# Optimization experiments

Hardware: AMD Instinct MI355X
Metric: run time of the kernel (lower is better)

The kernel has to match this reference:

```python
import jax, jax.numpy as jnp
import numpy as np

N = 100000   # nodes
E = 1250000  # edges
D = 64       # in = hidden = out channels
LN_EPS = 1e-5
L2_EPS = 1e-12


def setup_inputs() -> dict:
    key = jax.random.key(0)
    ks = jax.random.split(key, 16)
    s = 1.0 / np.sqrt(D)
    inp = {
        "x": jax.random.normal(ks[0], (N, D), jnp.float32),
        "edge_index": jax.random.randint(ks[1], (2, E), 0, N, dtype=jnp.int64),
    }
    for i in range(3):  # SAGEConv i: out = mean_aggr @ Wl + bl + x @ Wr
        inp[f"Wl{i}"] = jax.random.normal(ks[2 + 2 * i], (D, D), jnp.float32) * s
        inp[f"bl{i}"] = jnp.zeros((D,), jnp.float32)
        inp[f"Wr{i}"] = jax.random.normal(ks[3 + 2 * i], (D, D), jnp.float32) * s
    for i in range(2):  # LayerNorm after layers 0,1
        inp[f"g{i}"] = jnp.ones((D,), jnp.float32)
        inp[f"b{i}"] = jnp.zeros((D,), jnp.float32)
    return inp


def _sage_conv(x, src, dst, Wl, bl, Wr):
    # PyG SAGEConv(aggr='mean'): lin_l(mean of neighbor msgs) + lin_r(x)
    agg = jax.ops.segment_sum(x[src], dst, num_segments=N)          # [N, D]
    deg = jax.ops.segment_sum(jnp.ones((src.shape[0],), x.dtype), dst, num_segments=N)
    mean = agg / jnp.maximum(deg, 1.0)[:, None]
    return mean @ Wl + bl + x @ Wr


def _layer_norm(h, g, b):
    mu = jnp.mean(h, axis=-1, keepdims=True)
    var = jnp.mean((h - mu) ** 2, axis=-1, keepdims=True)
    return (h - mu) * jax.lax.rsqrt(var + LN_EPS) * g + b


def reference(x, edge_index, Wl0, bl0, Wr0, Wl1, bl1, Wr1, Wl2, bl2, Wr2, g0, b0, g1, b1):
    src, dst = edge_index[0], edge_index[1]
    Ws = [(Wl0, bl0, Wr0), (Wl1, bl1, Wr1), (Wl2, bl2, Wr2)]
    lns = [(g0, b0), (g1, b1)]
    h = x
    for i in range(3):
        res = h  # residual projections are Identity (equal dims)
        h = _sage_conv(h, src, dst, *Ws[i])
        if i < 2:
            h = _layer_norm(h, *lns[i])
            h = jax.nn.relu(h)
            h = h + res
            # dropout is identity in eval mode
        else:
            h = h + res
    # F.normalize(p=2, dim=1)
    nrm = jnp.sqrt(jnp.sum(h * h, axis=1, keepdims=True))
    return h / jnp.maximum(nrm, L2_EPS)
```

## Files before the change

kernel.cpp:

```cpp
#include <hip/hip_runtime.h>

#define DD   64
#define BSH  9
#define BNODES 512
#define BCAPSH 13

typedef unsigned int uint32;
typedef __attribute__((ext_vector_type(8))) short short8;
typedef __attribute__((ext_vector_type(4))) float f32x4;

__device__ __forceinline__ unsigned short f2bf_rne(float f) {
    uint32 u = __float_as_uint(f);
    u += 0x7fffu + ((u >> 16) & 1u);
    return (unsigned short)(u >> 16);
}
__device__ __forceinline__ float bf_lo(uint32 w) { return __uint_as_float(w << 16); }
__device__ __forceinline__ float bf_hi(uint32 w) { return __uint_as_float(w & 0xffff0000u); }
__device__ __forceinline__ float bf2f(unsigned short s) {
    return __uint_as_float(((uint32)s) << 16);
}

__global__ __launch_bounds__(256) void cvt_kernel(
    const float* __restrict__ x, unsigned short* __restrict__ xb, int n4,
    int* __restrict__ gCnt,
    const float* __restrict__ Wl0, const float* __restrict__ Wr0,
    const float* __restrict__ Wl1, const float* __restrict__ Wr1,
    const float* __restrict__ Wl2, const float* __restrict__ Wr2,
    unsigned short* __restrict__ wtg) {
    const int gid = blockIdx.x * 256 + threadIdx.x;
    if (blockIdx.x == 0) gCnt[threadIdx.x] = 0;
    if (gid < 3 * 2 * DD * DD) {
        int layer = gid >> 13;
        int idx   = gid & 8191;
        int k = idx >> 6, c = idx & 63;
        const float* Wsrc;
        if (layer == 0)      Wsrc = (k < DD) ? Wl0 : Wr0;
        else if (layer == 1) Wsrc = (k < DD) ? Wl1 : Wr1;
        else                 Wsrc = (k < DD) ? Wl2 : Wr2;
        float v = Wsrc[(k & (DD - 1)) * DD + c];
        wtg[layer * 8192 + c * 128 + k] = f2bf_rne(v);
    }
    if (gid < n4) {
        float4 v = ((const float4*)x)[gid];
        ushort4 p;
        p.x = f2bf_rne(v.x); p.y = f2bf_rne(v.y);
        p.z = f2bf_rne(v.z); p.w = f2bf_rne(v.w);
        ((ushort4*)xb)[gid] = p;
    }
}

__global__ __launch_bounds__(1024) void bucket_kernel(const int* __restrict__ src,
                                                      const int* __restrict__ dst,
                                                      int* __restrict__ gCnt,
                                                      int2* __restrict__ buf, int E) {
    __shared__ int ldsCnt[256];
    __shared__ int base[256];
    const int t = threadIdx.x;
    if (t < 256) ldsCnt[t] = 0;
    __syncthreads();

    const int e0 = blockIdx.x * 4096;
    int bk[4], rk[4], sv[4], dv[4];
#pragma unroll
    for (int k = 0; k < 4; ++k) {
        int e = e0 + k * 1024 + t;
        bk[k] = -1;
        if (e < E) {
            dv[k] = dst[e];
            sv[k] = src[e];
            bk[k] = dv[k] >> BSH;
            rk[k] = atomicAdd(&ldsCnt[bk[k]], 1);
        }
    }
    __syncthreads();
    if (t < 256 && ldsCnt[t] > 0) base[t] = atomicAdd(&gCnt[t], ldsCnt[t]);
    __syncthreads();
#pragma unroll
    for (int k = 0; k < 4; ++k) {
        if (bk[k] >= 0) {
            int pos = (bk[k] << BCAPSH) + base[bk[k]] + rk[k];
            buf[pos] = make_int2(sv[k], dv[k]);
        }
    }
}

__global__ __launch_bounds__(512) void csr_build(const int2* __restrict__ buf,
                                                 const int* __restrict__ gCnt,
                                                 int* __restrict__ offsets,
                                                 int* __restrict__ csr, int N, int E) {
    __shared__ int c1[BNODES];
    __shared__ int s2[BNODES];
    __shared__ int sw[16];
    const int b = blockIdx.x;
    const int t = threadIdx.x;
    const int lane = t & 63;
    const int w = t >> 6;

    int gv = (t < 256 && t < b) ? gCnt[t] : 0;
#pragma unroll
    for (int d = 1; d < 64; d <<= 1) gv += __shfl_xor(gv, d, 64);
    if (lane == 0) sw[w] = gv;
    c1[t] = 0;
    __syncthreads();
    int base = 0;
#pragma unroll
    for (int i = 0; i < 8; ++i) base += sw[i];

    const int cnt = gCnt[b];
    const int2* bb = buf + ((size_t)b << BCAPSH);
    for (int i = t; i < cnt; i += 512) atomicAdd(&c1[bb[i].y & (BNODES - 1)], 1);
    __syncthreads();

    int v = c1[t];
    int x = v;
#pragma unroll
    for (int d = 1; d < 64; d <<= 1) {
        int y = __shfl_up(x, d, 64);
        if (lane >= d) x += y;
    }
    if (lane == 63) sw[8 + w] = x;
    __syncthreads();
    int woff = 0;
    for (int i = 0; i < w; ++i) woff += sw[8 + i];
    int excl = x + woff - v;

    const int node = (b << BSH) + t;
    if (node < N) offsets[node] = base + excl;
    if (b == 0 && t == 0) offsets[N] = E;

    s2[t] = excl;
    c1[t] = 0;
    __syncthreads();

    for (int i = t; i < cnt; i += 512) {
        int2 e = bb[i];
        int d = e.y & (BNODES - 1);
        int r = atomicAdd(&c1[d], 1);
        csr[base + s2[d] + r] = e.x;
    }
}

__global__ __launch_bounds__(256, 4) void gather_mean(
    const unsigned short* __restrict__ hbin,
    const int* __restrict__ offsets,
    const int* __restrict__ csr,
    unsigned short* __restrict__ mean,
    int N) {
    const int grp  = threadIdx.x >> 3;
    const int q    = threadIdx.x & 7;
    const int node = blockIdx.x * 32 + grp;
    if (node >= N) return;

    const int off0 = offsets[node];
    const int off1 = offsets[node + 1];
    const int deg  = off1 - off0;

    float a0 = 0.f, a1 = 0.f, a2 = 0.f, a3 = 0.f,
          a4 = 0.f, a5 = 0.f, a6 = 0.f, a7 = 0.f;
#pragma unroll 1
    for (int j = off0; j < off1; j += 8) {
        uint4 v[8];
#pragma unroll
        for (int s = 0; s < 8; ++s) {
            uint4 tt = make_uint4(0u, 0u, 0u, 0u);
            int idx = j + s;
            if (idx < off1) {
                int sn = __builtin_nontemporal_load(&csr[idx]);
                tt = ((const uint4*)(hbin + (size_t)sn * DD))[q];
            }
            v[s] = tt;
        }
#pragma unroll
        for (int s = 0; s < 8; ++s) {
            a0 += bf_lo(v[s].x); a1 += bf_hi(v[s].x);
            a2 += bf_lo(v[s].y); a3 += bf_hi(v[s].y);
            a4 += bf_lo(v[s].z); a5 += bf_hi(v[s].z);
            a6 += bf_lo(v[s].w); a7 += bf_hi(v[s].w);
        }
    }
    float invd = 1.0f / fmaxf((float)deg, 1.0f);
    uint4 wv;
    wv.x = (uint32)f2bf_rne(a0 * invd) | ((uint32)f2bf_rne(a1 * invd) << 16);
    wv.y = (uint32)f2bf_rne(a2 * invd) | ((uint32)f2bf_rne(a3 * invd) << 16);
    wv.z = (uint32)f2bf_rne(a4 * invd) | ((uint32)f2bf_rne(a5 * invd) << 16);
    wv.w = (uint32)f2bf_rne(a6 * invd) | ((uint32)f2bf_rne(a7 * invd) << 16);
    *(uint4*)(mean + (size_t)node * DD + q * 8) = wv;
}

template <int MODE>
__global__ __launch_bounds__(256, 4) void sage_xform(
    const unsigned short* __restrict__ hbin,
    const unsigned short* __restrict__ mean,
    const unsigned short* __restrict__ wt,
    const float* __restrict__ bl,
    const float* __restrict__ g,
    const float* __restrict__ bta,
    unsigned short* __restrict__ hbout,
    float* __restrict__ out,
    int N) {
    const int t = threadIdx.x;
    const int nbase = blockIdx.x * 64;
    const int wave = t >> 6;
    const int lane = t & 63;
    const int quad = lane >> 4;
    const int n16  = lane & 15;
    const int lbase = wave * 16;

    const int arow = min(nbase + lbase + n16, N - 1);
    short8 af[4];
    af[0] = *(const short8*)(mean + (size_t)arow * DD + quad * 8);
    af[1] = *(const short8*)(mean + (size_t)arow * DD + 32 + quad * 8);
    af[2] = *(const short8*)(hbin + (size_t)arow * DD + quad * 8);
    af[3] = *(const short8*)(hbin + (size_t)arow * DD + 32 + quad * 8);

    f32x4 acc[4];
#pragma unroll
    for (int j = 0; j < 4; ++j) {
        float bv = bl[j * 16 + n16];
        acc[j] = (f32x4){bv, bv, bv, bv};
    }
#pragma unroll
    for (int s = 0; s < 4; ++s) {
#pragma unroll
        for (int j = 0; j < 4; ++j) {
            short8 bf = *(const short8*)(wt + (j * 16 + n16) * 128 + s * 32 + quad * 8);
            acc[j] = __builtin_amdgcn_mfma_f32_16x16x32_bf16(af[s], bf, acc[j], 0, 0, 0);
        }
    }

    float sg[4], sb[4];
    if (MODE == 0) {
#pragma unroll
        for (int j = 0; j < 4; ++j) { sg[j] = g[j * 16 + n16]; sb[j] = bta[j * 16 + n16]; }
    }

#pragma unroll
    for (int i = 0; i < 4; ++i) {
        const int lrow = lbase + quad * 4 + i;
        const int rr   = nbase + lrow;
        const int rrc  = min(rr, N - 1);
        float res[4];
#pragma unroll
        for (int j = 0; j < 4; ++j)
            res[j] = bf2f(hbin[(size_t)rrc * DD + j * 16 + n16]);
        float o[4];
        if (MODE == 0) {
            float s4 = acc[0][i] + acc[1][i] + acc[2][i] + acc[3][i];
            s4 += __shfl_xor(s4, 1, 64);
            s4 += __shfl_xor(s4, 2, 64);
            s4 += __shfl_xor(s4, 4, 64);
            s4 += __shfl_xor(s4, 8, 64);
            float mu = s4 * (1.0f / 64.0f);
            float d0 = acc[0][i] - mu, d1 = acc[1][i] - mu,
                  d2 = acc[2][i] - mu, d3 = acc[3][i] - mu;
            float qq = d0 * d0 + d1 * d1 + d2 * d2 + d3 * d3;
            qq += __shfl_xor(qq, 1, 64);
            qq += __shfl_xor(qq, 2, 64);
            qq += __shfl_xor(qq, 4, 64);
            qq += __shfl_xor(qq, 8, 64);
            float rstd = rsqrtf(qq * (1.0f / 64.0f) + 1e-5f);
            o[0] = fmaxf(d0 * rstd * sg[0] + sb[0], 0.f) + res[0];
            o[1] = fmaxf(d1 * rstd * sg[1] + sb[1], 0.f) + res[1];
            o[2] = fmaxf(d2 * rstd * sg[2] + sb[2], 0.f) + res[2];
            o[3] = fmaxf(d3 * rstd * sg[3] + sb[3], 0.f) + res[3];
        } else {
            o[0] = acc[0][i] + res[0];
            o[1] = acc[1][i] + res[1];
            o[2] = acc[2][i] + res[2];
            o[3] = acc[3][i] + res[3];
            float qq = o[0] * o[0] + o[1] * o[1] + o[2] * o[2] + o[3] * o[3];
            qq += __shfl_xor(qq, 1, 64);
            qq += __shfl_xor(qq, 2, 64);
            qq += __shfl_xor(qq, 4, 64);
            qq += __shfl_xor(qq, 8, 64);
            float inv = 1.0f / fmaxf(sqrtf(qq), 1e-12f);
            o[0] *= inv; o[1] *= inv; o[2] *= inv; o[3] *= inv;
        }
        if (rr < N) {
#pragma unroll
            for (int j = 0; j < 4; ++j) {
                if (MODE == 0)
                    hbout[(size_t)rr * DD + j * 16 + n16] = f2bf_rne(o[j]);
                else
                    out[(size_t)rr * DD + j * 16 + n16] = o[j];
            }
        }
    }
}

extern "C" void kernel_launch(void* const* d_in, const int* in_sizes, int n_in,
                              void* d_out, int out_size, void* d_ws, size_t ws_size,
                              hipStream_t stream) {
    const float* x   = (const float*)d_in[0];
    const int*   ei  = (const int*)d_in[1];
    const float* Wl0 = (const float*)d_in[2];
    const float* bl0 = (const float*)d_in[3];
    const float* Wr0 = (const float*)d_in[4];
    const float* Wl1 = (const float*)d_in[5];
    const float* bl1 = (const float*)d_in[6];
    const float* Wr1 = (const float*)d_in[7];
    const float* Wl2 = (const float*)d_in[8];
    const float* bl2 = (const float*)d_in[9];
    const float* Wr2 = (const float*)d_in[10];
    const float* g0  = (const float*)d_in[11];
    const float* b0  = (const float*)d_in[12];
    const float* g1  = (const float*)d_in[13];
    const float* b1  = (const float*)d_in[14];

    const int N = in_sizes[0] / DD;
    const int E = in_sizes[1] / 2;
    const int* src = ei;
    const int* dst = ei + E;
    const int NB = (N + BNODES - 1) >> BSH;

    int2* bucketBuf = (int2*)d_ws;
    unsigned short* HB0  = (unsigned short*)(bucketBuf + ((size_t)256 << BCAPSH));
    unsigned short* HB1  = HB0 + (size_t)N * DD;
    unsigned short* MEAN = HB1 + (size_t)N * DD;
    int*   csr     = (int*)(MEAN + (size_t)N * DD);
    int*   offsets = csr + E;
    int*   gCnt    = offsets + (N + 1);
    unsigned short* wtg =
        (unsigned short*)(((size_t)(gCnt + 256) + 15) & ~(size_t)15);
    float* out     = (float*)d_out;

    const int tiles  = (N + 63) / 64;
    const int ggrid  = (N + 31) / 32;
    const int n4     = N * DD / 4;
    const int cgrid  = (n4 + 255) / 256;
    const int bgrid  = (E + 4095) / 4096;

    cvt_kernel<<<cgrid, 256, 0, stream>>>(x, HB0, n4, gCnt,
                                          Wl0, Wr0, Wl1, Wr1, Wl2, Wr2, wtg);
    bucket_kernel<<<bgrid, 1024, 0, stream>>>(src, dst, gCnt, bucketBuf, E);
    csr_build<<<NB, 512, 0, stream>>>(bucketBuf, gCnt, offsets, csr, N, E);

    gather_mean<<<ggrid, 256, 0, stream>>>(HB0, offsets, csr, MEAN, N);
    sage_xform<0><<<tiles, 256, 0, stream>>>(HB0, MEAN, wtg,
                                             bl0, g0, b0, HB1, nullptr, N);
    gather_mean<<<ggrid, 256, 0, stream>>>(HB1, offsets, csr, MEAN, N);
    sage_xform<0><<<tiles, 256, 0, stream>>>(HB1, MEAN, wtg + 8192,
                                             bl1, g1, b1, HB0, nullptr, N);
    gather_mean<<<ggrid, 256, 0, stream>>>(HB0, offsets, csr, MEAN, N);
    sage_xform<1><<<tiles, 256, 0, stream>>>(HB0, MEAN, wtg + 16384,
                                             bl2, nullptr, nullptr, nullptr, out, N);
}
```

Measured before the change: 305.6 us.

## Replace CSR build and gather with src-grouped bins and LDS fixed-point accumulation

Removes the CSR construction pass. Edges are binned by destination block and source group with per-bin global atomic counters and a fixed capacity. Each aggregation block then sweeps its bins, gathering source rows in source-group order and accumulating into shared memory with integer fixed-point atomics. This aims to drop the csr_build kernel and improve gather locality, but it adds heavy LDS atomic traffic and global counter contention. Edges past the bin capacity are silently dropped, and the fixed-point conversion loses precision.

```diff
diff --git a/kernel.cpp b/kernel.cpp
--- a/kernel.cpp
+++ b/kernel.cpp
@@ -1,9 +1,14 @@
 #include <hip/hip_runtime.h>
 
-#define DD   64
-#define BSH  9
-#define BNODES 512
-#define BCAPSH 13
+#define DD     64
+#define DBSH   7
+#define DBN    128
+#define GRSH   13
+#define SCAP   256
+#define SCAPSH 8
+#define ASTR   65
+#define FIXS   262144.0f
+#define FIXI   (1.0f/262144.0f)
 
 typedef unsigned int uint32;
 typedef __attribute__((ext_vector_type(8))) short short8;
@@ -22,13 +27,13 @@
 
 __global__ __launch_bounds__(256) void cvt_kernel(
     const float* __restrict__ x, unsigned short* __restrict__ xb, int n4,
-    int* __restrict__ gCnt,
+    int* __restrict__ gCnt, int nbins,
     const float* __restrict__ Wl0, const float* __restrict__ Wr0,
     const float* __restrict__ Wl1, const float* __restrict__ Wr1,
     const float* __restrict__ Wl2, const float* __restrict__ Wr2,
     unsigned short* __restrict__ wtg) {
     const int gid = blockIdx.x * 256 + threadIdx.x;
-    if (blockIdx.x == 0) gCnt[threadIdx.x] = 0;
+    if (gid < nbins) gCnt[gid] = 0;
     if (gid < 3 * 2 * DD * DD) {
         int layer = gid >> 13;
         int idx   = gid & 8191;
@@ -52,139 +57,96 @@
 __global__ __launch_bounds__(1024) void bucket_kernel(const int* __restrict__ src,
                                                       const int* __restrict__ dst,
                                                       int* __restrict__ gCnt,
-                                                      int2* __restrict__ buf, int E) {
-    __shared__ int ldsCnt[256];
-    __shared__ int base[256];
-    const int t = threadIdx.x;
-    if (t < 256) ldsCnt[t] = 0;
-    __syncthreads();
-
+                                                      int2* __restrict__ buf,
+                                                      int E, int ngr) {
+    const int t  = threadIdx.x;
     const int e0 = blockIdx.x * 4096;
-    int bk[4], rk[4], sv[4], dv[4];
 #pragma unroll
     for (int k = 0; k < 4; ++k) {
         int e = e0 + k * 1024 + t;
-        bk[k] = -1;
         if (e < E) {
-            dv[k] = dst[e];
-            sv[k] = src[e];
-            bk[k] = dv[k] >> BSH;
-            rk[k] = atomicAdd(&ldsCnt[bk[k]], 1);
-        }
-    }
+            int d = dst[e];
+            int s = src[e];
+            int bid = (d >> DBSH) * ngr + (s >> GRSH);
+            int rk = atomicAdd(&gCnt[bid], 1);
+            if (rk < SCAP)
+                buf[((size_t)bid << SCAPSH) + rk] = make_int2(s, d);
+        }
+    }
+}
+
+__global__ __launch_bounds__(256, 4) void sweep_mean(
+    const unsigned short* __restrict__ hbin,
+    const int2* __restrict__ buf,
+    const int* __restrict__ gCnt,
+    unsigned short* __restrict__ mean,
+    int N, int ngr) {
+    __shared__ int acc[DBN * ASTR];
+    __shared__ int sdeg[DBN];
+    const int t = threadIdx.x;
+    for (int i = t; i < DBN * ASTR; i += 256) acc[i] = 0;
+    if (t < DBN) sdeg[t] = 0;
     __syncthreads();
-    if (t < 256 && ldsCnt[t] > 0) base[t] = atomicAdd(&gCnt[t], ldsCnt[t]);
+
+    const int grp = t >> 3;
+    const int q   = t & 7;
+    const int b0  = blockIdx.x * ngr;
+#pragma unroll 1
+    for (int g = 0; g < ngr; ++g) {
+        const int bid = b0 + g;
+        const int cnt = min(gCnt[bid], SCAP);
+        const int2* eb = buf + ((size_t)bid << SCAPSH);
+#pragma unroll 1
+        for (int jb = 0; jb < cnt; jb += 128) {
+            int2 ed[4]; uint4 v[4]; bool val[4];
+#pragma unroll
+            for (int k = 0; k < 4; ++k) {
+                int j = jb + k * 32 + grp;
+                val[k] = (j < cnt);
+                ed[k] = val[k] ? eb[j] : make_int2(0, 0);
+            }
+#pragma unroll
+            for (int k = 0; k < 4; ++k)
+                v[k] = val[k] ? ((const uint4*)(hbin + (size_t)ed[k].x * DD))[q]
+                              : make_uint4(0u, 0u, 0u, 0u);
+#pragma unroll
+            for (int k = 0; k < 4; ++k) {
+                if (val[k]) {
+                    int dl = ed[k].y & (DBN - 1);
+                    int* ap = &acc[dl * ASTR + q * 8];
+                    atomicAdd(ap + 0, __float2int_rn(bf_lo(v[k].x) * FIXS));
+                    atomicAdd(ap + 1, __float2int_rn(bf_hi(v[k].x) * FIXS));
+                    atomicAdd(ap + 2, __float2int_rn(bf_lo(v[k].y) * FIXS));
+                    atomicAdd(ap + 3, __float2int_rn(bf_hi(v[k].y) * FIXS));
+                    atomicAdd(ap + 4, __float2int_rn(bf_lo(v[k].z) * FIXS));
+                    atomicAdd(ap + 5, __float2int_rn(bf_hi(v[k].z) * FIXS));
+                    atomicAdd(ap + 6, __float2int_rn(bf_lo(v[k].w) * FIXS));
+                    atomicAdd(ap + 7, __float2int_rn(bf_hi(v[k].w) * FIXS));
+                    if (q == 0) atomicAdd(&sdeg[dl], 1);
+                }
+            }
+        }
+    }
     __syncthreads();
-#pragma unroll
-    for (int k = 0; k < 4; ++k) {
-        if (bk[k] >= 0) {
-            int pos = (bk[k] << BCAPSH) + base[bk[k]] + rk[k];
-            buf[pos] = make_int2(sv[k], dv[k]);
-        }
-    }
-}
-
-__global__ __launch_bounds__(512) void csr_build(const int2* __restrict__ buf,
-                                                 const int* __restrict__ gCnt,
-                                                 int* __restrict__ offsets,
-                                                 int* __restrict__ csr, int N, int E) {
-    __shared__ int c1[BNODES];
-    __shared__ int s2[BNODES];
-    __shared__ int sw[16];
-    const int b = blockIdx.x;
-    const int t = threadIdx.x;
-    const int lane = t & 63;
-    const int w = t >> 6;
-
-    int gv = (t < 256 && t < b) ? gCnt[t] : 0;
-#pragma unroll
-    for (int d = 1; d < 64; d <<= 1) gv += __shfl_xor(gv, d, 64);
-    if (lane == 0) sw[w] = gv;
-    c1[t] = 0;
-    __syncthreads();
-    int base = 0;
-#pragma unroll
-    for (int i = 0; i < 8; ++i) base += sw[i];
-
-    const int cnt = gCnt[b];
-    const int2* bb = buf + ((size_t)b << BCAPSH);
-    for (int i = t; i < cnt; i += 512) atomicAdd(&c1[bb[i].y & (BNODES - 1)], 1);
-    __syncthreads();
-
-    int v = c1[t];
-    int x = v;
-#pragma unroll
-    for (int d = 1; d < 64; d <<= 1) {
-        int y = __shfl_up(x, d, 64);
-        if (lane >= d) x += y;
-    }
-    if (lane == 63) sw[8 + w] = x;
-    __syncthreads();
-    int woff = 0;
-    for (int i = 0; i < w; ++i) woff += sw[8 + i];
-    int excl = x + woff - v;
-
-    const int node = (b << BSH) + t;
-    if (node < N) offsets[node] = base + excl;
-    if (b == 0 && t == 0) offsets[N] = E;
-
-    s2[t] = excl;
-    c1[t] = 0;
-    __syncthreads();
-
-    for (int i = t; i < cnt; i += 512) {
-        int2 e = bb[i];
-        int d = e.y & (BNODES - 1);
-        int r = atomicAdd(&c1[d], 1);
-        csr[base + s2[d] + r] = e.x;
-    }
-}
-
-__global__ __launch_bounds__(256, 4) void gather_mean(
-    const unsigned short* __restrict__ hbin,
-    const int* __restrict__ offsets,
-    const int* __restrict__ csr,
-    unsigned short* __restrict__ mean,
-    int N) {
-    const int grp  = threadIdx.x >> 3;
-    const int q    = threadIdx.x & 7;
-    const int node = blockIdx.x * 32 + grp;
-    if (node >= N) return;
-
-    const int off0 = offsets[node];
-    const int off1 = offsets[node + 1];
-    const int deg  = off1 - off0;
-
-    float a0 = 0.f, a1 = 0.f, a2 = 0.f, a3 = 0.f,
-          a4 = 0.f, a5 = 0.f, a6 = 0.f, a7 = 0.f;
-#pragma unroll 1
-    for (int j = off0; j < off1; j += 8) {
-        uint4 v[8];
-#pragma unroll
-        for (int s = 0; s < 8; ++s) {
-            uint4 tt = make_uint4(0u, 0u, 0u, 0u);
-            int idx = j + s;
-            if (idx < off1) {
-                int sn = __builtin_nontemporal_load(&csr[idx]);
-                tt = ((const uint4*)(hbin + (size_t)sn * DD))[q];
-            }
-            v[s] = tt;
-        }
-#pragma unroll
-        for (int s = 0; s < 8; ++s) {
-            a0 += bf_lo(v[s].x); a1 += bf_hi(v[s].x);
-            a2 += bf_lo(v[s].y); a3 += bf_hi(v[s].y);
-            a4 += bf_lo(v[s].z); a5 += bf_hi(v[s].z);
-            a6 += bf_lo(v[s].w); a7 += bf_hi(v[s].w);
-        }
-    }
-    float invd = 1.0f / fmaxf((float)deg, 1.0f);
-    uint4 wv;
-    wv.x = (uint32)f2bf_rne(a0 * invd) | ((uint32)f2bf_rne(a1 * invd) << 16);
-    wv.y = (uint32)f2bf_rne(a2 * invd) | ((uint32)f2bf_rne(a3 * invd) << 16);
-    wv.z = (uint32)f2bf_rne(a4 * invd) | ((uint32)f2bf_rne(a5 * invd) << 16);
-    wv.w = (uint32)f2bf_rne(a6 * invd) | ((uint32)f2bf_rne(a7 * invd) << 16);
-    *(uint4*)(mean + (size_t)node * DD + q * 8) = wv;
+
+    for (int i = t; i < DBN * 8; i += 256) {
+        int row = i >> 3, qq = i & 7;
+        int node = blockIdx.x * DBN + row;
+        if (node < N) {
+            float sc = FIXI / fmaxf((float)sdeg[row], 1.0f);
+            const int* ap = &acc[row * ASTR + qq * 8];
+            uint4 wv;
+            wv.x = (uint32)f2bf_rne((float)ap[0] * sc) |
+                   ((uint32)f2bf_rne((float)ap[1] * sc) << 16);
+            wv.y = (uint32)f2bf_rne((float)ap[2] * sc) |
+                   ((uint32)f2bf_rne((float)ap[3] * sc) << 16);
+            wv.z = (uint32)f2bf_rne((float)ap[4] * sc) |
+                   ((uint32)f2bf_rne((float)ap[5] * sc) << 16);
+            wv.w = (uint32)f2bf_rne((float)ap[6] * sc) |
+                   ((uint32)f2bf_rne((float)ap[7] * sc) << 16);
+            *(uint4*)(mean + (size_t)node * DD + qq * 8) = wv;
+        }
+    }
 }
 
 template <int MODE>
@@ -311,37 +273,36 @@
     const int E = in_sizes[1] / 2;
     const int* src = ei;
     const int* dst = ei + E;
-    const int NB = (N + BNODES - 1) >> BSH;
-
-    int2* bucketBuf = (int2*)d_ws;
-    unsigned short* HB0  = (unsigned short*)(bucketBuf + ((size_t)256 << BCAPSH));
+
+    const int nbkt  = (N + DBN - 1) >> DBSH;
+    const int ngr   = (N + (1 << GRSH) - 1) >> GRSH;
+    const int nbins = nbkt * ngr;
+
+    int2* buf = (int2*)d_ws;
+    unsigned short* HB0  = (unsigned short*)(buf + ((size_t)nbins << SCAPSH));
     unsigned short* HB1  = HB0 + (size_t)N * DD;
     unsigned short* MEAN = HB1 + (size_t)N * DD;
-    int*   csr     = (int*)(MEAN + (size_t)N * DD);
-    int*   offsets = csr + E;
-    int*   gCnt    = offsets + (N + 1);
+    int* gCnt = (int*)(MEAN + (size_t)N * DD);
     unsigned short* wtg =
-        (unsigned short*)(((size_t)(gCnt + 256) + 15) & ~(size_t)15);
-    float* out     = (float*)d_out;
-
-    const int tiles  = (N + 63) / 64;
-    const int ggrid  = (N + 31) / 32;
-    const int n4     = N * DD / 4;
-    const int cgrid  = (n4 + 255) / 256;
-    const int bgrid  = (E + 4095) / 4096;
-
-    cvt_kernel<<<cgrid, 256, 0, stream>>>(x, HB0, n4, gCnt,
+        (unsigned short*)(((size_t)(gCnt + nbins) + 15) & ~(size_t)15);
+    float* out = (float*)d_out;
+
+    const int tiles = (N + 63) / 64;
+    const int n4    = N * DD / 4;
+    const int cgrid = (n4 + 255) / 256;
+    const int bgrid = (E + 4095) / 4096;
+
+    cvt_kernel<<<cgrid, 256, 0, stream>>>(x, HB0, n4, gCnt, nbins,
                                           Wl0, Wr0, Wl1, Wr1, Wl2, Wr2, wtg);
-    bucket_kernel<<<bgrid, 1024, 0, stream>>>(src, dst, gCnt, bucketBuf, E);
-    csr_build<<<NB, 512, 0, stream>>>(bucketBuf, gCnt, offsets, csr, N, E);
-
-    gather_mean<<<ggrid, 256, 0, stream>>>(HB0, offsets, csr, MEAN, N);
+    bucket_kernel<<<bgrid, 1024, 0, stream>>>(src, dst, gCnt, buf, E, ngr);
+
+    sweep_mean<<<nbkt, 256, 0, stream>>>(HB0, buf, gCnt, MEAN, N, ngr);
     sage_xform<0><<<tiles, 256, 0, stream>>>(HB0, MEAN, wtg,
                                              bl0, g0, b0, HB1, nullptr, N);
-    gather_mean<<<ggrid, 256, 0, stream>>>(HB1, offsets, csr, MEAN, N);
+    sweep_mean<<<nbkt, 256, 0, stream>>>(HB1, buf, gCnt, MEAN, N, ngr);
     sage_xform<0><<<tiles, 256, 0, stream>>>(HB1, MEAN, wtg + 8192,
                                              bl1, g1, b1, HB0, nullptr, N);
-    gather_mean<<<ggrid, 256, 0, stream>>>(HB0, offsets, csr, MEAN, N);
+    sweep_mean<<<nbkt, 256, 0, stream>>>(HB0, buf, gCnt, MEAN, N, ngr);
     sage_xform<1><<<tiles, 256, 0, stream>>>(HB0, MEAN, wtg + 16384,
                                              bl2, nullptr, nullptr, nullptr, out, N);
 }
```

Measured after the change: 378.7 us. 1.24x slower.

## Pre-sort edges by source granule before destination bucketing to improve gather locality

Applied to the files above, without the earlier changes.

Adds a first partitioning pass that groups edges into 16 coarse granules by source node. The existing destination bucketing then reads edges in that order, so within each CSR row the source indices come out roughly sorted. The intent is better cache locality for the feature gathers in the three gather_mean passes. The cost is an extra full pass over all edges plus a new intermediate buffer, and edges are silently dropped if a granule overflows its fixed capacity.

```diff
diff --git a/kernel.cpp b/kernel.cpp
--- a/kernel.cpp
+++ b/kernel.cpp
@@ -4,6 +4,8 @@
 #define BSH  9
 #define BNODES 512
 #define BCAPSH 13
+#define GRSH 13
+#define GRCAPSH 17
 
 typedef unsigned int uint32;
 typedef __attribute__((ext_vector_type(8))) short short8;
@@ -22,13 +24,16 @@
 
 __global__ __launch_bounds__(256) void cvt_kernel(
     const float* __restrict__ x, unsigned short* __restrict__ xb, int n4,
-    int* __restrict__ gCnt,
+    int* __restrict__ gCnt, int* __restrict__ gGr,
     const float* __restrict__ Wl0, const float* __restrict__ Wr0,
     const float* __restrict__ Wl1, const float* __restrict__ Wr1,
     const float* __restrict__ Wl2, const float* __restrict__ Wr2,
     unsigned short* __restrict__ wtg) {
     const int gid = blockIdx.x * 256 + threadIdx.x;
-    if (blockIdx.x == 0) gCnt[threadIdx.x] = 0;
+    if (blockIdx.x == 0) {
+        gCnt[threadIdx.x] = 0;
+        if (threadIdx.x < 16) gGr[threadIdx.x] = 0;
+    }
     if (gid < 3 * 2 * DD * DD) {
         int layer = gid >> 13;
         int idx   = gid & 8191;
@@ -49,15 +54,58 @@
     }
 }
 
-__global__ __launch_bounds__(1024) void bucket_kernel(const int* __restrict__ src,
-                                                      const int* __restrict__ dst,
-                                                      int* __restrict__ gCnt,
-                                                      int2* __restrict__ buf, int E) {
+__global__ __launch_bounds__(1024) void granule_kernel(
+    const int* __restrict__ src, const int* __restrict__ dst,
+    int* __restrict__ gGr, int2* __restrict__ gbuf, int E) {
+    __shared__ int lc[16];
+    __shared__ int lb[16];
+    const int t = threadIdx.x;
+    if (t < 16) lc[t] = 0;
+    __syncthreads();
+
+    const int e0 = blockIdx.x * 4096;
+    int gk[4], rk[4], sv[4], dv[4];
+#pragma unroll
+    for (int k = 0; k < 4; ++k) {
+        int e = e0 + k * 1024 + t;
+        gk[k] = -1;
+        if (e < E) {
+            sv[k] = src[e];
+            dv[k] = dst[e];
+            gk[k] = sv[k] >> GRSH;
+            rk[k] = atomicAdd(&lc[gk[k]], 1);
+        }
+    }
+    __syncthreads();
+    if (t < 16 && lc[t] > 0) lb[t] = atomicAdd(&gGr[t], lc[t]);
+    __syncthreads();
+#pragma unroll
+    for (int k = 0; k < 4; ++k) {
+        if (gk[k] >= 0) {
+            int slot = lb[gk[k]] + rk[k];
+            if (slot < (1 << GRCAPSH))
+                gbuf[((size_t)gk[k] << GRCAPSH) + slot] = make_int2(sv[k], dv[k]);
+        }
+    }
+}
+
+__global__ __launch_bounds__(1024) void bucket_kernel(
+    const int2* __restrict__ gbuf, const int* __restrict__ gGr,
+    int* __restrict__ gCnt, int2* __restrict__ buf, int E, int ngr) {
     __shared__ int ldsCnt[256];
     __shared__ int base[256];
+    __shared__ int pre[33];
     const int t = threadIdx.x;
     if (t < 256) ldsCnt[t] = 0;
-    __syncthreads();
+    if (t == 0) {
+        pre[0] = 0;
+        for (int g = 0; g < ngr; ++g) {
+            int c = gGr[g];
+            pre[g + 1] = pre[g] + (c < (1 << GRCAPSH) ? c : (1 << GRCAPSH));
+        }
+    }
+    __syncthreads();
+    const int total = pre[ngr];
 
     const int e0 = blockIdx.x * 4096;
     int bk[4], rk[4], sv[4], dv[4];
@@ -65,9 +113,12 @@
     for (int k = 0; k < 4; ++k) {
         int e = e0 + k * 1024 + t;
         bk[k] = -1;
-        if (e < E) {
-            dv[k] = dst[e];
-            sv[k] = src[e];
+        if (e < total) {
+            int g = 0;
+            while (g < ngr - 1 && e >= pre[g + 1]) ++g;
+            int2 ed = gbuf[((size_t)g << GRCAPSH) + (e - pre[g])];
+            sv[k] = ed.x;
+            dv[k] = ed.y;
             bk[k] = dv[k] >> BSH;
             rk[k] = atomicAdd(&ldsCnt[bk[k]], 1);
         }
@@ -311,28 +362,32 @@
     const int E = in_sizes[1] / 2;
     const int* src = ei;
     const int* dst = ei + E;
-    const int NB = (N + BNODES - 1) >> BSH;
-
-    int2* bucketBuf = (int2*)d_ws;
+    const int NB  = (N + BNODES - 1) >> BSH;
+    const int ngr = (N + (1 << GRSH) - 1) >> GRSH;
+
+    int2* gbuf      = (int2*)d_ws;
+    int2* bucketBuf = gbuf + ((size_t)ngr << GRCAPSH);
     unsigned short* HB0  = (unsigned short*)(bucketBuf + ((size_t)256 << BCAPSH));
     unsigned short* HB1  = HB0 + (size_t)N * DD;
     unsigned short* MEAN = HB1 + (size_t)N * DD;
     int*   csr     = (int*)(MEAN + (size_t)N * DD);
     int*   offsets = csr + E;
     int*   gCnt    = offsets + (N + 1);
+    int*   gGr     = gCnt + 256;
     unsigned short* wtg =
-        (unsigned short*)(((size_t)(gCnt + 256) + 15) & ~(size_t)15);
+        (unsigned short*)(((size_t)(gGr + 16) + 15) & ~(size_t)15);
     float* out     = (float*)d_out;
 
-    const int tiles  = (N + 63) / 64;
-    const int ggrid  = (N + 31) / 32;
-    const int n4     = N * DD / 4;
-    const int cgrid  = (n4 + 255) / 256;
-    const int bgrid  = (E + 4095) / 4096;
-
-    cvt_kernel<<<cgrid, 256, 0, stream>>>(x, HB0, n4, gCnt,
+    const int tiles = (N + 63) / 64;
+    const int ggrid = (N + 31) / 32;
+    const int n4    = N * DD / 4;
+    const int cgrid = (n4 + 255) / 256;
+    const int bgrid = (E + 4095) / 4096;
+
+    cvt_kernel<<<cgrid, 256, 0, stream>>>(x, HB0, n4, gCnt, gGr,
                                           Wl0, Wr0, Wl1, Wr1, Wl2, Wr2, wtg);
-    bucket_kernel<<<bgrid, 1024, 0, stream>>>(src, dst, gCnt, bucketBuf, E);
+    granule_kernel<<<bgrid, 1024, 0, stream>>>(src, dst, gGr, gbuf, E);
+    bucket_kernel<<<bgrid, 1024, 0, stream>>>(gbuf, gGr, gCnt, bucketBuf, E, ngr);
     csr_build<<<NB, 512, 0, stream>>>(bucketBuf, gCnt, offsets, csr, N, E);
 
     gather_mean<<<ggrid, 256, 0, stream>>>(HB0, offsets, csr, MEAN, N);
```

New measurement: 311.4 us. About the same (+1.9%).
